# Performance work log

Hardware: AMD Instinct MI355X
Metric: run time of the kernel (lower is better)

## Reference

```python
import jax, jax.numpy as jnp
import numpy as np

B, T, D, H, R = 16, 2048, 512, 1024, 16


def setup_inputs() -> dict:
    key = jax.random.key(0)
    ks = jax.random.split(key, 8)
    s = lambda d: 1.0 / np.sqrt(d)
    return {
        "x": jax.random.normal(ks[0], (B, T, D), jnp.float32),
        "Wx": jax.random.normal(ks[1], (D, H), jnp.float32) * s(D),
        "Wh": jax.random.normal(ks[2], (H, H), jnp.float32) * s(H),
        "Wq": jax.random.normal(ks[3], (D, R), jnp.float32) * s(D),
        "Wk": jax.random.normal(ks[4], (D, R), jnp.float32) * s(D),
        "Wv": jax.random.normal(ks[5], (D, H), jnp.float32) * s(D),
        "Wd": jax.random.normal(ks[6], (D, 1), jnp.float32) * s(D),
        "b": jnp.zeros((H,), jnp.float32),
        "bd": jnp.ones((1,), jnp.float32),
    }


def reference(x, Wx, Wh, Wq, Wk, Wv, Wd, b, bd):
    """DREAM fast-weight RNN.

    Per step: decay lambda_t = sigmoid(x_t Wd + bd)  (B,1)
              F_t = lambda_t * F_{t-1} + v_t k_t^T   (B,H,R) outer-product memory
              r_t = F_t q_t                          (B,H)   fast-weight read
              h_t = tanh(x_t Wx + h_{t-1} Wh + r_t + b)
    """
    Bsz = x.shape[0]
    Hd, Rk = Wv.shape[1], Wq.shape[1]
    # Precompute all time-parallel projections once (big GEMMs outside the scan).
    q = jnp.einsum('btd,dr->btr', x, Wq)            # (B,T,R)
    k = jnp.einsum('btd,dr->btr', x, Wk)            # (B,T,R)
    v = jnp.einsum('btd,dh->bth', x, Wv)            # (B,T,H)
    lam = jax.nn.sigmoid(jnp.einsum('btd,do->bto', x, Wd) + bd)  # (B,T,1)
    xw = jnp.einsum('btd,dh->bth', x, Wx)           # (B,T,H)

    h0 = jnp.zeros((Bsz, Hd), x.dtype)
    F0 = jnp.zeros((Bsz, Hd, Rk), x.dtype)

    def step(carry, inp):
        h, F = carry
        q_t, k_t, v_t, lam_t, xw_t = inp
        F = lam_t[:, :, None] * F + v_t[:, :, None] * k_t[:, None, :]  # (B,H,R)
        read = jnp.einsum('bhr,br->bh', F, q_t)
        h = jnp.tanh(xw_t + h @ Wh + read + b)
        return (h, F), h

    # scan over time axis
    inps = (q.transpose(1, 0, 2), k.transpose(1, 0, 2), v.transpose(1, 0, 2),
            lam.transpose(1, 0, 2), xw.transpose(1, 0, 2))
    (h_fin, F_fin), hs = jax.lax.scan(step, (h0, F0), inps)
    output = hs.transpose(1, 0, 2)  # (B,T,H)
    return output, h_fin, F_fin
```

## Files before the change

kernel.cpp:

```cpp
#include <hip/hip_runtime.h>
#include <math.h>

#define Bc 16
#define Tc 2048
#define Dc 512
#define Hc 1024
#define Rc 16

__global__ __launch_bounds__(256) void gemm_xw(const float* __restrict__ X,
                                               const float* __restrict__ W,
                                               float* __restrict__ out)
{
    __shared__ float As[16][128];
    __shared__ float Bs[16][64];
    const int tid = threadIdx.x;
    const int m0 = blockIdx.x * 128;
    const int n0 = blockIdx.y * 64;
    const int tx = tid & 15, ty = tid >> 4;
    const int am = tid >> 2, ak = (tid & 3) * 4;
    const int bk = tid >> 4, bn = (tid & 15) * 4;
    float acc[8][4] = {};
    for (int k0 = 0; k0 < 512; k0 += 16) {
        if (k0) __syncthreads();
        float4 a0 = *(const float4*)&X[(size_t)(m0 + am) * 512 + k0 + ak];
        float4 a1 = *(const float4*)&X[(size_t)(m0 + am + 64) * 512 + k0 + ak];
        float4 bv = *(const float4*)&W[(size_t)(k0 + bk) * 1024 + n0 + bn];
        As[ak + 0][am] = a0.x; As[ak + 1][am] = a0.y;
        As[ak + 2][am] = a0.z; As[ak + 3][am] = a0.w;
        As[ak + 0][am + 64] = a1.x; As[ak + 1][am + 64] = a1.y;
        As[ak + 2][am + 64] = a1.z; As[ak + 3][am + 64] = a1.w;
        *(float4*)&Bs[bk][bn] = bv;
        __syncthreads();
        #pragma unroll
        for (int kk = 0; kk < 16; ++kk) {
            float4 x0 = *(const float4*)&As[kk][ty * 8];
            float4 x1 = *(const float4*)&As[kk][ty * 8 + 4];
            float4 y  = *(const float4*)&Bs[kk][tx * 4];
            float a[8] = {x0.x, x0.y, x0.z, x0.w, x1.x, x1.y, x1.z, x1.w};
            float bb[4] = {y.x, y.y, y.z, y.w};
            #pragma unroll
            for (int i = 0; i < 8; ++i)
                #pragma unroll
                for (int j = 0; j < 4; ++j)
                    acc[i][j] += a[i] * bb[j];
        }
    }
    #pragma unroll
    for (int i = 0; i < 8; ++i) {
        float4 r;
        r.x = acc[i][0]; r.y = acc[i][1]; r.z = acc[i][2]; r.w = acc[i][3];
        *(float4*)&out[(size_t)(m0 + ty * 8 + i) * 1024 + n0 + tx * 4] = r;
    }
}

__global__ __launch_bounds__(256) void qkl_kernel(const float* __restrict__ X,
    const float* __restrict__ Wq, const float* __restrict__ Wk,
    const float* __restrict__ Wd, const float* __restrict__ bd,
    float* __restrict__ q, float* __restrict__ k, float* __restrict__ lam)
{
    __shared__ float xs[8 * 512];
    const int tid = threadIdx.x;
    const size_t row0 = (size_t)blockIdx.x * 8;
    #pragma unroll
    for (int c = 0; c < 4; ++c) {
        int f = (c * 256 + tid) * 4;
        *(float4*)&xs[f] = *(const float4*)&X[row0 * 512 + f];
    }
    __syncthreads();
    for (int t = tid; t < 264; t += 256) {
        int r = t / 33, c = t - r * 33;
        const float* xr = &xs[r * 512];
        const float* Wp; int ldw;
        if (c < 16)      { Wp = Wq + c;        ldw = 16; }
        else if (c < 32) { Wp = Wk + (c - 16); ldw = 16; }
        else             { Wp = Wd;            ldw = 1;  }
        float s = 0.f;
        for (int kk = 0; kk < 512; ++kk) s += xr[kk] * Wp[(size_t)kk * ldw];
        if (c < 16)      q[(row0 + r) * 16 + c] = s;
        else if (c < 32) k[(row0 + r) * 16 + (c - 16)] = s;
        else             lam[row0 + r] = 1.f / (1.f + expf(-(s + bd[0])));
    }
}

__global__ __launch_bounds__(256, 1) void rec_fused(
    const float* __restrict__ Wh, const float* __restrict__ qg,
    const float* __restrict__ kg, const float* __restrict__ vg,
    const float* __restrict__ lamg, const float* __restrict__ bias,
    float* __restrict__ out0, float* __restrict__ hfin,
    float* __restrict__ Ffin, float* __restrict__ hbuf,
    int* __restrict__ xcc_tab)
{
    __shared__ float hs[2 * 1152];
    __shared__ float red2[2][256];
    __shared__ float pre_lds[2][64];
    __shared__ float F_lds[64][17];

    const int tid = threadIdx.x;
    const int bid = blockIdx.x;
    const int g = bid & 7, sl = bid >> 3;
    const int c0 = sl * 32;
    const int kp = tid >> 3;
    const int cu = tid & 7;
    const int wv = tid >> 6;

    const int my_xcc = __builtin_amdgcn_s_getreg(63508) & 0xF;
    if (tid == 0) {
        int val = my_xcc + 1;
        int* tp = xcc_tab + bid;
        asm volatile("global_store_dword %0, %1, off sc0 sc1"
                     :: "v"(tp), "v"(val) : "memory");
    }

    float wr[128];
    #pragma unroll
    for (int i = 0; i < 32; ++i) {
        float4 w4 = *(const float4*)&Wh[(size_t)(kp * 32 + i) * 1024 + c0 + cu * 4];
        wr[i * 4 + 0] = w4.x; wr[i * 4 + 1] = w4.y;
        wr[i * 4 + 2] = w4.z; wr[i * 4 + 3] = w4.w;
    }

    const int sb_ = tid >> 7;
    const int f   = (tid & 127) * 8;
    float* stage_base = &hs[sb_ * 1152 + (f >> 5) * 36 + (f & 31)];

    int fastf;
    {
        const int prod_bid = (f >> 5) * 8 + g;
        const int* tp = xcc_tab + prod_bid;
        int tv;
        for (;;) {
            asm volatile("global_load_dword %0, %1, off sc0 sc1\n\t"
                         "s_waitcnt vmcnt(0)"
                         : "=&v"(tv) : "v"(tp) : "memory");
            if (tv != -1) break;
        }
        fastf = ((tv - 1) == my_xcc) ? 1 : 0;
    }

    const int j64 = tid & 63;
    const int fb = j64 >> 5, fci = j64 & 31;
    const int bg = g * 2 + fb;
    const bool isScan = (tid >= 192);
    const bool isFin  = (tid < 64);

    float bias_r = 0.f, plam = 0.f, pv = 0.f, pxw = 0.f;
    float4 pq[4], pk4[4];
    if (isScan) {
        bias_r = bias[c0 + fci];
        #pragma unroll
        for (int r = 0; r < 16; ++r) F_lds[j64][r] = 0.f;
        const size_t row = (size_t)bg * Tc;
        plam = lamg[row];
        pv   = vg[row * Hc + c0 + fci];
        pxw  = out0[row * Hc + c0 + fci];
        const float* qp  = qg + row * 16;
        const float* kpp = kg + row * 16;
        #pragma unroll
        for (int r4 = 0; r4 < 4; ++r4) {
            pq[r4]  = *(const float4*)(qp + r4 * 4);
            pk4[r4] = *(const float4*)(kpp + r4 * 4);
        }
    }

    for (int t = 0; t < Tc; ++t) {
        const int buf = t & 1;
        float* h_rd = hbuf + (t & 1) * (16 * 1024) + g * 2048;
        float* h_wr = hbuf + ((t + 1) & 1) * (16 * 1024) + g * 2048;
        const float off_r = ((t >> 1) & 1) ? 4.0f : 0.0f;
        const float off_w = (((t + 1) >> 1) & 1) ? 4.0f : 0.0f;

        if (isScan) {
            float rd = 0.f;
            #pragma unroll
            for (int r4 = 0; r4 < 4; ++r4) {
                float f0 = F_lds[j64][r4 * 4 + 0];
                float f1 = F_lds[j64][r4 * 4 + 1];
                float f2 = F_lds[j64][r4 * 4 + 2];
                float f3 = F_lds[j64][r4 * 4 + 3];
                f0 = plam * f0 + pv * pk4[r4].x; rd += f0 * pq[r4].x;
                f1 = plam * f1 + pv * pk4[r4].y; rd += f1 * pq[r4].y;
                f2 = plam * f2 + pv * pk4[r4].z; rd += f2 * pq[r4].z;
                f3 = plam * f3 + pv * pk4[r4].w; rd += f3 * pq[r4].w;
                F_lds[j64][r4 * 4 + 0] = f0;
                F_lds[j64][r4 * 4 + 1] = f1;
                F_lds[j64][r4 * 4 + 2] = f2;
                F_lds[j64][r4 * 4 + 3] = f3;
            }
            pre_lds[buf][j64] = pxw + rd + bias_r;
            if (t == Tc - 1) {
                #pragma unroll
                for (int r = 0; r < 16; ++r)
                    Ffin[((size_t)bg * Hc + c0 + fci) * 16 + r] = F_lds[j64][r];
            } else {
                const size_t row = (size_t)bg * Tc + (t + 1);
                plam = lamg[row];
                pv   = vg[row * Hc + c0 + fci];
                pxw  = out0[row * Hc + c0 + fci];
                const float* qp  = qg + row * 16;
                const float* kpp = kg + row * 16;
                #pragma unroll
                for (int r4 = 0; r4 < 4; ++r4) {
                    pq[r4]  = *(const float4*)(qp + r4 * 4);
                    pk4[r4] = *(const float4*)(kpp + r4 * 4);
                }
            }
        }

        if (t > 0) {
            const float lo = off_r - 1.5f, hi = off_r + 1.5f;
            const float* p0 = h_rd + sb_ * 1024 + f;
            const float* p1 = p0 + 4;
            float4 r0, r1;
            int tries = 0;
            for (;;) {
                if (fastf) {
                    asm volatile(
                        "global_load_dwordx4 %0, %2, off sc0\n\t"
                        "global_load_dwordx4 %1, %3, off sc0\n\t"
                        "s_waitcnt vmcnt(0)"
                        : "=&v"(r0), "=&v"(r1)
                        : "v"(p0), "v"(p1) : "memory");
                } else {
                    asm volatile(
                        "global_load_dwordx4 %0, %2, off sc0 sc1\n\t"
                        "global_load_dwordx4 %1, %3, off sc0 sc1\n\t"
                        "s_waitcnt vmcnt(0)"
                        : "=&v"(r0), "=&v"(r1)
                        : "v"(p0), "v"(p1) : "memory");
                }
                bool ok = r0.x > lo && r0.x < hi && r0.y > lo && r0.y < hi
                       && r0.z > lo && r0.z < hi && r0.w > lo && r0.w < hi
                       && r1.x > lo && r1.x < hi && r1.y > lo && r1.y < hi
                       && r1.z > lo && r1.z < hi && r1.w > lo && r1.w < hi;
                if (ok) break;
                if (fastf && ++tries > 64) fastf = 0;
            }
            r0.x -= off_r; r0.y -= off_r; r0.z -= off_r; r0.w -= off_r;
            r1.x -= off_r; r1.y -= off_r; r1.z -= off_r; r1.w -= off_r;
            *(float4*)(stage_base)     = r0;
            *(float4*)(stage_base + 4) = r1;
        } else {
            float4 z = {0.f, 0.f, 0.f, 0.f};
            *(float4*)(stage_base)     = z;
            *(float4*)(stage_base + 4) = z;
        }
        __syncthreads();

        float acc[8];
        #pragma unroll
        for (int z = 0; z < 8; ++z) acc[z] = 0.f;
        #pragma unroll
        for (int bb = 0; bb < 2; ++bb) {
            const float* hb = &hs[bb * 1152 + kp * 36];
            #pragma unroll
            for (int i = 0; i < 8; ++i) {
                float4 h4 = *(const float4*)(hb + i * 4);
                #pragma unroll
                for (int j = 0; j < 4; ++j)
                    acc[j * 2 + bb] += h4.x * wr[(i * 4 + 0) * 4 + j]
                                     + h4.y * wr[(i * 4 + 1) * 4 + j]
                                     + h4.z * wr[(i * 4 + 2) * 4 + j]
                                     + h4.w * wr[(i * 4 + 3) * 4 + j];
            }
        }

        #pragma unroll
        for (int z = 0; z < 8; ++z) {
            float s = acc[z];
            s += __shfl_xor(s, 8);
            s += __shfl_xor(s, 16);
            s += __shfl_xor(s, 32);
            acc[z] = s;
        }
        if (j64 < 8) {
            float4 ra, rb;
            ra.x = acc[0]; ra.y = acc[1]; ra.z = acc[2]; ra.w = acc[3];
            rb.x = acc[4]; rb.y = acc[5]; rb.z = acc[6]; rb.w = acc[7];
            *(float4*)&red2[buf][wv * 64 + j64 * 8]     = ra;
            *(float4*)&red2[buf][wv * 64 + j64 * 8 + 4] = rb;
        }
        __syncthreads();

        if (isFin) {
            const int cu_f = fci >> 2, jf = fci & 3;
            const int z = jf * 2 + fb;
            float tot = pre_lds[buf][j64];
            #pragma unroll
            for (int ww = 0; ww < 4; ++ww)
                tot += red2[buf][ww * 64 + cu_f * 8 + z];
            float hv = tanhf(tot);
            float sv = hv + off_w;
            float* hp = h_wr + fb * 1024 + c0 + fci;
            asm volatile(
                "global_store_dword %0, %1, off sc0 sc1"
                :: "v"(hp), "v"(sv) : "memory");
            size_t oidx = ((size_t)bg * Tc + t) * Hc + c0 + fci;
            out0[oidx] = hv;
            if (t == Tc - 1) hfin[(size_t)bg * Hc + c0 + fci] = hv;
        }
    }
}

extern "C" void kernel_launch(void* const* d_in, const int* in_sizes, int n_in,
                              void* d_out, int out_size, void* d_ws, size_t ws_size,
                              hipStream_t stream)
{
    const float* x    = (const float*)d_in[0];
    const float* Wx   = (const float*)d_in[1];
    const float* Wh   = (const float*)d_in[2];
    const float* Wq   = (const float*)d_in[3];
    const float* Wk   = (const float*)d_in[4];
    const float* Wv   = (const float*)d_in[5];
    const float* Wd   = (const float*)d_in[6];
    const float* bias = (const float*)d_in[7];
    const float* bd   = (const float*)d_in[8];

    float* out0 = (float*)d_out;
    float* hfin = out0 + (size_t)Bc * Tc * Hc;
    float* Ffin = hfin + (size_t)Bc * Hc;

    float* wsf  = (float*)d_ws;
    float* v    = wsf;
    float* q    = v + (size_t)Bc * Tc * Hc;
    float* k    = q + (size_t)Bc * Tc * Rc;
    float* lam  = k + (size_t)Bc * Tc * Rc;
    float* hbuf = lam + (size_t)Bc * Tc;
    int*   xcc  = (int*)(hbuf + 2 * (size_t)Bc * Hc);

    hipMemsetAsync(hbuf, 0x7F, 2 * (size_t)Bc * Hc * sizeof(float), stream);
    hipMemsetAsync(xcc, 0xFF, 256 * sizeof(int), stream);

    dim3 gg(256, 16);
    gemm_xw<<<gg, 256, 0, stream>>>(x, Wx, out0);
    gemm_xw<<<gg, 256, 0, stream>>>(x, Wv, v);
    qkl_kernel<<<4096, 256, 0, stream>>>(x, Wq, Wk, Wd, bd, q, k, lam);
    rec_fused<<<256, 256, 0, stream>>>(Wh, q, k, v, lam, bias,
                                       out0, hfin, Ffin, hbuf, xcc);
}
```

Baseline: 7.531 ms.

## Repartition Wh per wave to drop cross-wave LDS reduction and barrier

Each wave now owns 8 output columns and splits the K dimension across its 64 lanes (16 rows each), so the full reduction runs inside the wave with a recursive-halving shuffle. This removes the red2 LDS buffer and the second __syncthreads per timestep. The h staging buffer is double-buffered with a padded 17-stride layout to avoid bank conflicts. Each finishing lane also issues an extra sc0 store in addition to the sc0 sc1 store, and the fast-path retry limit is raised. The risk is that the extra store and more shuffles add latency on the serial critical path, and that removing the barrier depends on correct double buffering of pre_lds and hs.

```diff
diff --git a/kernel.cpp b/kernel.cpp
--- a/kernel.cpp
+++ b/kernel.cpp
@@ -90,8 +90,7 @@
     float* __restrict__ Ffin, float* __restrict__ hbuf,
     int* __restrict__ xcc_tab)
 {
-    __shared__ float hs[2 * 1152];
-    __shared__ float red2[2][256];
+    __shared__ float hs[2][2 * 1088];
     __shared__ float pre_lds[2][64];
     __shared__ float F_lds[64][17];
 
@@ -99,8 +98,7 @@
     const int bid = blockIdx.x;
     const int g = bid & 7, sl = bid >> 3;
     const int c0 = sl * 32;
-    const int kp = tid >> 3;
-    const int cu = tid & 7;
+    const int lane = tid & 63;
     const int wv = tid >> 6;
 
     const int my_xcc = __builtin_amdgcn_s_getreg(63508) & 0xF;
@@ -113,15 +111,19 @@
 
     float wr[128];
     #pragma unroll
-    for (int i = 0; i < 32; ++i) {
-        float4 w4 = *(const float4*)&Wh[(size_t)(kp * 32 + i) * 1024 + c0 + cu * 4];
-        wr[i * 4 + 0] = w4.x; wr[i * 4 + 1] = w4.y;
-        wr[i * 4 + 2] = w4.z; wr[i * 4 + 3] = w4.w;
+    for (int i = 0; i < 16; ++i) {
+        const float* wp = &Wh[(size_t)(lane * 16 + i) * 1024 + c0 + wv * 8];
+        float4 wa = *(const float4*)wp;
+        float4 wb = *(const float4*)(wp + 4);
+        wr[i * 8 + 0] = wa.x; wr[i * 8 + 1] = wa.y;
+        wr[i * 8 + 2] = wa.z; wr[i * 8 + 3] = wa.w;
+        wr[i * 8 + 4] = wb.x; wr[i * 8 + 5] = wb.y;
+        wr[i * 8 + 6] = wb.z; wr[i * 8 + 7] = wb.w;
     }
 
     const int sb_ = tid >> 7;
     const int f   = (tid & 127) * 8;
-    float* stage_base = &hs[sb_ * 1152 + (f >> 5) * 36 + (f & 31)];
+    const int physb = (f >> 4) * 17 + (f & 15);
 
     int fastf;
     {
@@ -138,21 +140,20 @@
     }
 
     const int j64 = tid & 63;
-    const int fb = j64 >> 5, fci = j64 & 31;
-    const int bg = g * 2 + fb;
+    const int sb = j64 >> 5, sci = j64 & 31;
+    const int sbg = g * 2 + sb;
     const bool isScan = (tid >= 192);
-    const bool isFin  = (tid < 64);
 
     float bias_r = 0.f, plam = 0.f, pv = 0.f, pxw = 0.f;
     float4 pq[4], pk4[4];
     if (isScan) {
-        bias_r = bias[c0 + fci];
+        bias_r = bias[c0 + sci];
         #pragma unroll
         for (int r = 0; r < 16; ++r) F_lds[j64][r] = 0.f;
-        const size_t row = (size_t)bg * Tc;
+        const size_t row = (size_t)sbg * Tc;
         plam = lamg[row];
-        pv   = vg[row * Hc + c0 + fci];
-        pxw  = out0[row * Hc + c0 + fci];
+        pv   = vg[row * Hc + c0 + sci];
+        pxw  = out0[row * Hc + c0 + sci];
         const float* qp  = qg + row * 16;
         const float* kpp = kg + row * 16;
         #pragma unroll
@@ -161,6 +162,11 @@
             pk4[r4] = *(const float4*)(kpp + r4 * 4);
         }
     }
+
+    const bool hb5 = (lane & 32) != 0;
+    const bool hb4 = (lane & 16) != 0;
+    const bool hb3 = (lane & 8)  != 0;
+    const bool hb2 = (lane & 4)  != 0;
 
     for (int t = 0; t < Tc; ++t) {
         const int buf = t & 1;
@@ -190,12 +196,12 @@
             if (t == Tc - 1) {
                 #pragma unroll
                 for (int r = 0; r < 16; ++r)
-                    Ffin[((size_t)bg * Hc + c0 + fci) * 16 + r] = F_lds[j64][r];
+                    Ffin[((size_t)sbg * Hc + c0 + sci) * 16 + r] = F_lds[j64][r];
             } else {
-                const size_t row = (size_t)bg * Tc + (t + 1);
+                const size_t row = (size_t)sbg * Tc + (t + 1);
                 plam = lamg[row];
-                pv   = vg[row * Hc + c0 + fci];
-                pxw  = out0[row * Hc + c0 + fci];
+                pv   = vg[row * Hc + c0 + sci];
+                pxw  = out0[row * Hc + c0 + sci];
                 const float* qp  = qg + row * 16;
                 const float* kpp = kg + row * 16;
                 #pragma unroll
@@ -206,97 +212,108 @@
             }
         }
 
-        if (t > 0) {
-            const float lo = off_r - 1.5f, hi = off_r + 1.5f;
-            const float* p0 = h_rd + sb_ * 1024 + f;
-            const float* p1 = p0 + 4;
-            float4 r0, r1;
-            int tries = 0;
-            for (;;) {
-                if (fastf) {
-                    asm volatile(
-                        "global_load_dwordx4 %0, %2, off sc0\n\t"
-                        "global_load_dwordx4 %1, %3, off sc0\n\t"
-                        "s_waitcnt vmcnt(0)"
-                        : "=&v"(r0), "=&v"(r1)
-                        : "v"(p0), "v"(p1) : "memory");
-                } else {
-                    asm volatile(
-                        "global_load_dwordx4 %0, %2, off sc0 sc1\n\t"
-                        "global_load_dwordx4 %1, %3, off sc0 sc1\n\t"
-                        "s_waitcnt vmcnt(0)"
-                        : "=&v"(r0), "=&v"(r1)
-                        : "v"(p0), "v"(p1) : "memory");
+        {
+            float* sp = &hs[buf][sb_ * 1088 + physb];
+            if (t > 0) {
+                const float lo = off_r - 1.5f, hi = off_r + 1.5f;
+                const float* p0 = h_rd + sb_ * 1024 + f;
+                const float* p1 = p0 + 4;
+                float4 r0, r1;
+                int tries = 0;
+                for (;;) {
+                    if (fastf) {
+                        asm volatile(
+                            "global_load_dwordx4 %0, %2, off sc0\n\t"
+                            "global_load_dwordx4 %1, %3, off sc0\n\t"
+                            "s_waitcnt vmcnt(0)"
+                            : "=&v"(r0), "=&v"(r1)
+                            : "v"(p0), "v"(p1) : "memory");
+                    } else {
+                        asm volatile(
+                            "global_load_dwordx4 %0, %2, off sc0 sc1\n\t"
+                            "global_load_dwordx4 %1, %3, off sc0 sc1\n\t"
+                            "s_waitcnt vmcnt(0)"
+                            : "=&v"(r0), "=&v"(r1)
+                            : "v"(p0), "v"(p1) : "memory");
+                    }
+                    bool ok = r0.x > lo && r0.x < hi && r0.y > lo && r0.y < hi
+                           && r0.z > lo && r0.z < hi && r0.w > lo && r0.w < hi
+                           && r1.x > lo && r1.x < hi && r1.y > lo && r1.y < hi
+                           && r1.z > lo && r1.z < hi && r1.w > lo && r1.w < hi;
+                    if (ok) break;
+                    if (fastf && ++tries > 256) fastf = 0;
                 }
-                bool ok = r0.x > lo && r0.x < hi && r0.y > lo && r0.y < hi
-                       && r0.z > lo && r0.z < hi && r0.w > lo && r0.w < hi
-                       && r1.x > lo && r1.x < hi && r1.y > lo && r1.y < hi
-                       && r1.z > lo && r1.z < hi && r1.w > lo && r1.w < hi;
-                if (ok) break;
-                if (fastf && ++tries > 64) fastf = 0;
+                r0.x -= off_r; r0.y -= off_r; r0.z -= off_r; r0.w -= off_r;
+                r1.x -= off_r; r1.y -= off_r; r1.z -= off_r; r1.w -= off_r;
+                *(float4*)(sp)     = r0;
+                *(float4*)(sp + 4) = r1;
+            } else {
+                float4 z = {0.f, 0.f, 0.f, 0.f};
+                *(float4*)(sp)     = z;
+                *(float4*)(sp + 4) = z;
             }
-            r0.x -= off_r; r0.y -= off_r; r0.z -= off_r; r0.w -= off_r;
-            r1.x -= off_r; r1.y -= off_r; r1.z -= off_r; r1.w -= off_r;
-            *(float4*)(stage_base)     = r0;
-            *(float4*)(stage_base + 4) = r1;
-        } else {
-            float4 z = {0.f, 0.f, 0.f, 0.f};
-            *(float4*)(stage_base)     = z;
-            *(float4*)(stage_base + 4) = z;
         }
         __syncthreads();
 
-        float acc[8];
-        #pragma unroll
-        for (int z = 0; z < 8; ++z) acc[z] = 0.f;
+        float acc[16];
+        #pragma unroll
+        for (int z = 0; z < 16; ++z) acc[z] = 0.f;
         #pragma unroll
         for (int bb = 0; bb < 2; ++bb) {
-            const float* hb = &hs[bb * 1152 + kp * 36];
+            const float* hb = &hs[buf][bb * 1088 + lane * 17];
             #pragma unroll
-            for (int i = 0; i < 8; ++i) {
-                float4 h4 = *(const float4*)(hb + i * 4);
+            for (int e = 0; e < 4; ++e) {
+                float4 h4 = *(const float4*)(hb + e * 4);
                 #pragma unroll
-                for (int j = 0; j < 4; ++j)
-                    acc[j * 2 + bb] += h4.x * wr[(i * 4 + 0) * 4 + j]
-                                     + h4.y * wr[(i * 4 + 1) * 4 + j]
-                                     + h4.z * wr[(i * 4 + 2) * 4 + j]
-                                     + h4.w * wr[(i * 4 + 3) * 4 + j];
+                for (int cc = 0; cc < 8; ++cc)
+                    acc[cc * 2 + bb] += h4.x * wr[(e * 4 + 0) * 8 + cc]
+                                      + h4.y * wr[(e * 4 + 1) * 8 + cc]
+                                      + h4.z * wr[(e * 4 + 2) * 8 + cc]
+                                      + h4.w * wr[(e * 4 + 3) * 8 + cc];
             }
         }
 
+        float s8[8];
         #pragma unroll
         for (int z = 0; z < 8; ++z) {
-            float s = acc[z];
-            s += __shfl_xor(s, 8);
-            s += __shfl_xor(s, 16);
-            s += __shfl_xor(s, 32);
-            acc[z] = s;
-        }
-        if (j64 < 8) {
-            float4 ra, rb;
-            ra.x = acc[0]; ra.y = acc[1]; ra.z = acc[2]; ra.w = acc[3];
-            rb.x = acc[4]; rb.y = acc[5]; rb.z = acc[6]; rb.w = acc[7];
-            *(float4*)&red2[buf][wv * 64 + j64 * 8]     = ra;
-            *(float4*)&red2[buf][wv * 64 + j64 * 8 + 4] = rb;
-        }
-        __syncthreads();
-
-        if (isFin) {
-            const int cu_f = fci >> 2, jf = fci & 3;
-            const int z = jf * 2 + fb;
-            float tot = pre_lds[buf][j64];
-            #pragma unroll
-            for (int ww = 0; ww < 4; ++ww)
-                tot += red2[buf][ww * 64 + cu_f * 8 + z];
+            float keep = hb5 ? acc[8 + z] : acc[z];
+            float send = hb5 ? acc[z] : acc[8 + z];
+            s8[z] = keep + __shfl_xor(send, 32);
+        }
+        float s4[4];
+        #pragma unroll
+        for (int z = 0; z < 4; ++z) {
+            float keep = hb4 ? s8[4 + z] : s8[z];
+            float send = hb4 ? s8[z] : s8[4 + z];
+            s4[z] = keep + __shfl_xor(send, 16);
+        }
+        float s2[2];
+        #pragma unroll
+        for (int z = 0; z < 2; ++z) {
+            float keep = hb3 ? s4[2 + z] : s4[z];
+            float send = hb3 ? s4[z] : s4[2 + z];
+            s2[z] = keep + __shfl_xor(send, 8);
+        }
+        float v1k = (hb2 ? s2[1] : s2[0]) + __shfl_xor(hb2 ? s2[0] : s2[1], 4);
+        v1k += __shfl_xor(v1k, 2);
+        v1k += __shfl_xor(v1k, 1);
+
+        if ((lane & 3) == 0) {
+            const int z  = lane >> 2;
+            const int cc = z >> 1, bb = z & 1;
+            const int ci = wv * 8 + cc;
+            const int bg2 = g * 2 + bb;
+            float tot = v1k + pre_lds[buf][bb * 32 + ci];
             float hv = tanhf(tot);
             float sv = hv + off_w;
-            float* hp = h_wr + fb * 1024 + c0 + fci;
-            asm volatile(
-                "global_store_dword %0, %1, off sc0 sc1"
-                :: "v"(hp), "v"(sv) : "memory");
-            size_t oidx = ((size_t)bg * Tc + t) * Hc + c0 + fci;
+            float* hp = h_wr + bb * 1024 + c0 + ci;
+            asm volatile("global_store_dword %0, %1, off sc0"
+                         :: "v"(hp), "v"(sv) : "memory");
+            asm volatile("global_store_dword %0, %1, off sc0 sc1"
+                         :: "v"(hp), "v"(sv) : "memory");
+            size_t oidx = ((size_t)bg2 * Tc + t) * Hc + c0 + ci;
             out0[oidx] = hv;
-            if (t == Tc - 1) hfin[(size_t)bg * Hc + c0 + fci] = hv;
+            if (t == Tc - 1) hfin[(size_t)bg2 * Hc + c0 + ci] = hv;
         }
     }
 }
```

Result: slower. 13.74 ms (+82.4%).
